# Kernel optimization log

Measured on AMD Instinct MI355X. Metric: run time of the kernel, lower is better.

Reference implementation:

```python
import jax, jax.numpy as jnp
import numpy as np

N = 10000      # num_nodes
E = 80000      # num_edges (no self-loops; added in reference like PyG GATConv)
DIN, DH, DOUT = 768, 256, 64
EPS = 1e-16


def _gat_conv(x, src, dst, W, a_src, a_dst, b, heads, out_ch):
    """PyG-style GATConv (concat=True, negative_slope=0.2, eval mode).
    x: [n, in]; src/dst: [e] (self-loops already included); W: [in, heads*out_ch];
    a_src/a_dst: [heads, out_ch]; b: [heads*out_ch]. Returns [n, heads*out_ch]."""
    n = x.shape[0]
    h = (x @ W).reshape(n, heads, out_ch)                 # [n, H, C]
    e = jax.nn.leaky_relu((h * a_src).sum(-1)[src] + (h * a_dst).sum(-1)[dst],
                          negative_slope=0.2)             # [e, H]
    m = jax.ops.segment_max(e, dst, num_segments=n)       # [n, H]
    m = jnp.where(jnp.isfinite(m), m, 0.0)                # guard empty segments
    p = jnp.exp(e - m[dst])                               # [e, H]
    denom = jax.ops.segment_sum(p, dst, num_segments=n)   # [n, H]
    alpha = p / (denom[dst] + EPS)                        # [e, H]
    msg = h[src] * alpha[:, :, None]                      # [e, H, C]  (largest buffer)
    out = jax.ops.segment_sum(msg, dst, num_segments=n)   # [n, H, C]
    return out.reshape(n, heads * out_ch) + b


def setup_inputs() -> dict:
    key = jax.random.key(0)
    ks = jax.random.split(key, 20)

    def lin(k, fan_in, fan_out):
        return jax.random.normal(k, (fan_in, fan_out), jnp.float32) / np.sqrt(fan_in)

    x = jax.random.normal(ks[0], (N, DIN), jnp.float32)
    src = jax.random.randint(ks[1], (E,), 0, N)
    off = jax.random.randint(ks[2], (E,), 1, N)
    dst = (src + off) % N                                  # guarantees no self-loops
    edge_index = jnp.stack([src, dst]).astype(jnp.int64)

    inp = {"x": x, "edge_index": edge_index}
    inp["W1"]  = lin(ks[3], DIN, 8 * DH)
    inp["as1"] = jax.random.normal(ks[4], (8, DH), jnp.float32) / np.sqrt(DH)
    inp["ad1"] = jax.random.normal(ks[5], (8, DH), jnp.float32) / np.sqrt(DH)
    inp["b1"]  = jnp.zeros((8 * DH,), jnp.float32)
    inp["W2"]  = lin(ks[6], 8 * DH, 4 * DH)
    inp["as2"] = jax.random.normal(ks[7], (4, DH), jnp.float32) / np.sqrt(DH)
    inp["ad2"] = jax.random.normal(ks[8], (4, DH), jnp.float32) / np.sqrt(DH)
    inp["b2"]  = jnp.zeros((4 * DH,), jnp.float32)
    inp["W3"]  = lin(ks[9], 4 * DH, DOUT)
    inp["as3"] = jax.random.normal(ks[10], (1, DOUT), jnp.float32) / np.sqrt(DOUT)
    inp["ad3"] = jax.random.normal(ks[11], (1, DOUT), jnp.float32) / np.sqrt(DOUT)
    inp["b3"]  = jnp.zeros((DOUT,), jnp.float32)
    # reasoning MLP: 64 -> 256 -> 128 -> 1
    inp["r1w"] = lin(ks[12], DOUT, DH);      inp["r1b"] = jnp.zeros((DH,), jnp.float32)
    inp["r2w"] = lin(ks[13], DH, DH // 2);   inp["r2b"] = jnp.zeros((DH // 2,), jnp.float32)
    inp["r3w"] = lin(ks[14], DH // 2, 1);    inp["r3b"] = jnp.zeros((1,), jnp.float32)
    return inp


def reference(x, edge_index, W1, as1, ad1, b1, W2, as2, ad2, b2,
              W3, as3, ad3, b3, r1w, r1b, r2w, r2b, r3w, r3b):
    n = x.shape[0]
    loops = jnp.arange(n, dtype=edge_index.dtype)
    src = jnp.concatenate([edge_index[0], loops])
    dst = jnp.concatenate([edge_index[1], loops])
    # dropout layers are identity in eval mode
    x1 = jax.nn.elu(_gat_conv(x,  src, dst, W1, as1, ad1, b1, 8, DH))
    x2 = jax.nn.elu(_gat_conv(x1, src, dst, W2, as2, ad2, b2, 4, DH))
    x3 = _gat_conv(x2, src, dst, W3, as3, ad3, b3, 1, DOUT)
    h = jax.nn.relu(x3 @ r1w + r1b)
    h = jax.nn.relu(h @ r2w + r2b)
    node_scores = h @ r3w + r3b                            # [n, 1]
    return node_scores, x3
```

## Files before the change

### kernel.cpp

```cpp
#include <hip/hip_runtime.h>
#include <stdint.h>

typedef unsigned short u16;
using s16x8 = __attribute__((ext_vector_type(8))) short;
using f32x4 = __attribute__((ext_vector_type(4))) float;
using u16x8 = __attribute__((ext_vector_type(8))) unsigned short;
using u16x4 = __attribute__((ext_vector_type(4))) unsigned short;

#define DEVINL __device__ __forceinline__

DEVINL float b2f(u16 u) { return __uint_as_float(((uint32_t)u) << 16); }
DEVINL u16 f2b(float f) {
  uint32_t x = __float_as_uint(f);
  return (u16)((x + 0x7fffu + ((x >> 16) & 1u)) >> 16);
}
DEVINL float ldf(const void* p, size_t i, int isbf) {
  return isbf ? b2f(((const u16*)p)[i]) : ((const float*)p)[i];
}
DEVINL void stf(void* p, size_t i, int isbf, float v) {
  if (isbf) ((u16*)p)[i] = f2b(v);
  else      ((float*)p)[i] = v;
}

typedef __attribute__((address_space(1))) const void gvoid;
typedef __attribute__((address_space(3))) void lvoid;
DEVINL void gload_lds16(const u16* g, u16* l) {
  __builtin_amdgcn_global_load_lds((gvoid*)g, (lvoid*)l, 16, 0, 0);
}

constexpr int NN = 10000;
constexpr int NE = 80000;
constexpr int NTOT = 90000;

__global__ void detect_kernel(const void* __restrict__ x, int* __restrict__ flag) {
  int lane = threadIdx.x;
  u16 w = ((const u16*)x)[lane * 97 + 13];
  int e = (w >> 7) & 0xFF;
  int sane = (e >= 0x50 && e <= 0x8A) ? 1 : 0;
  unsigned long long b = __ballot(sane);
  if (lane == 0) flag[0] = (__popcll(b) >= 56) ? 1 : 0;
}

__global__ void cvt_kernel(const void* __restrict__ in, u16* __restrict__ out,
                           int n, const int* __restrict__ FLAG) {
  int isbf = *FLAG;
  int i = blockIdx.x * 256 + threadIdx.x;
  if (i >= n) return;
  out[i] = isbf ? ((const u16*)in)[i] : f2b(((const float*)in)[i]);
}

struct TD { const void* in; u16* out; int R, C, t0; };
struct TD5 { TD d[5]; };
__global__ void transpose_all(TD5 td, const int* __restrict__ FLAG) {
  int isbf = *FLAG;
  __shared__ float tile[32][33];
  int t = blockIdx.x;
  int k = 0;
#pragma unroll
  for (int j = 1; j < 5; j++) if (t >= td.d[j].t0) k = j;
  const void* in = td.d[k].in;
  u16* out = td.d[k].out;
  int R = td.d[k].R, C = td.d[k].C;
  int tl = t - td.d[k].t0;
  int tcols = C / 32;
  int bx = (tl % tcols) * 32, by = (tl / tcols) * 32;
  int tx = threadIdx.x, ty = threadIdx.y;
  for (int j = 0; j < 32; j += 8) {
    int r = by + ty + j, c = bx + tx;
    tile[ty + j][tx] = ldf(in, (size_t)r * C + c, isbf);
  }
  __syncthreads();
  for (int j = 0; j < 32; j += 8) {
    int r = bx + ty + j, c = by + tx;
    out[(size_t)r * R + c] = f2b(tile[tx][ty + j]);
  }
}

__global__ void init_kernel(int* __restrict__ deg, float* __restrict__ hz, int nz) {
  int i = blockIdx.x * blockDim.x + threadIdx.x;
  if (i < NN) deg[i] = 1;
  if (i < nz) hz[i] = 0.f;
}

__global__ void count_deg_kernel(const int* __restrict__ ei, int* __restrict__ deg) {
  int e = blockIdx.x * blockDim.x + threadIdx.x;
  if (e < NE) atomicAdd(&deg[ei[NE + e]], 1);
}

__global__ __launch_bounds__(1024) void scan_kernel(const int* __restrict__ deg,
                                                    int* __restrict__ offs,
                                                    int* __restrict__ cursor, int n) {
  __shared__ int wsum[16];
  __shared__ int carry_s;
  int tid = threadIdx.x, lane = tid & 63, wid = tid >> 6;
  if (tid == 0) carry_s = 0;
  __syncthreads();
  for (int base = 0; base < n; base += 1024) {
    int idx = base + tid;
    int v = (idx < n) ? deg[idx] : 0;
    int s = v;
#pragma unroll
    for (int o = 1; o < 64; o <<= 1) { int t = __shfl_up(s, o); if (lane >= o) s += t; }
    if (lane == 63) wsum[wid] = s;
    __syncthreads();
    if (wid == 0) {
      int w = (lane < 16) ? wsum[lane] : 0;
#pragma unroll
      for (int o = 1; o < 16; o <<= 1) { int t = __shfl_up(w, o); if (lane >= o) w += t; }
      if (lane < 16) wsum[lane] = w;
    }
    __syncthreads();
    int inc = s + (wid > 0 ? wsum[wid - 1] : 0) + carry_s;
    if (idx < n) { offs[idx + 1] = inc; cursor[idx] = inc - v; }
    __syncthreads();
    if (tid == 0) carry_s += wsum[15];
    __syncthreads();
  }
  if (tid == 0) offs[0] = 0;
}

__global__ void scatter_kernel(const int* __restrict__ ei, int* __restrict__ cursor,
                               int* __restrict__ csr_src) {
  int e = blockIdx.x * blockDim.x + threadIdx.x;
  if (e >= NTOT) return;
  int s, d;
  if (e < NE) { s = ei[e]; d = ei[NE + e]; }
  else        { s = e - NE; d = s; }
  int pos = atomicAdd(&cursor[d], 1);
  csr_src[pos] = s;
}

template <int BM, int BN, int WM, int WN>
__global__ __launch_bounds__(256) void gemm_kernel(const u16* __restrict__ A,
                                                   const u16* __restrict__ Bt,
                                                   u16* __restrict__ C,
                                                   int M, int K, int N, int nN,
                                                   const void* __restrict__ bias,
                                                   int do_relu,
                                                   const void* __restrict__ asrc,
                                                   const void* __restrict__ adst,
                                                   float* __restrict__ hs,
                                                   float* __restrict__ hd,
                                                   int H, int Cc,
                                                   const int* __restrict__ FLAG) {
  constexpr int BK = 64;
  constexpr int WTM = BM / WM, WTN = BN / WN;
  constexpr int FM = WTM / 16, FN = WTN / 16;
  constexpr int ACH = BM / 32;
  constexpr int BCH = BN / 32;

  __shared__ u16 smem[(BM + BN) * BK];
  u16* lA = smem;
  u16* lB = smem + BM * BK;

  int tid = threadIdx.x;
  int lane = tid & 63, wid = tid >> 6;
  int wm = wid / WN, wn = wid % WN;
  int isbf = (bias || asrc) ? *FLAG : 0;

  int nwg = gridDim.x;
  int q = nwg >> 3, r = nwg & 7;
  int xcd = blockIdx.x & 7, pos = blockIdx.x >> 3;
  int wgid = (xcd < r ? xcd * (q + 1) : r * (q + 1) + (xcd - r) * q) + pos;
  int bm0 = (wgid / nN) * BM, bn0 = (wgid % nN) * BN;

  int srow = lane >> 3;
  int scol = ((lane & 7) ^ (lane >> 3)) << 3;

  f32x4 acc[FM][FN];
#pragma unroll
  for (int m = 0; m < FM; m++)
#pragma unroll
    for (int n = 0; n < FN; n++) acc[m][n] = (f32x4){0.f, 0.f, 0.f, 0.f};

  for (int k0 = 0; k0 < K; k0 += BK) {
#pragma unroll
    for (int i = 0; i < ACH; i++) {
      int c = wid * ACH + i;
      int row = c * 8 + srow;
      int grow = bm0 + row;
      if (grow > M - 1) grow = M - 1;
      gload_lds16(A + (size_t)grow * K + k0 + scol, lA + c * 512);
    }
#pragma unroll
    for (int i = 0; i < BCH; i++) {
      int c = wid * BCH + i;
      int row = c * 8 + srow;
      gload_lds16(Bt + (size_t)(bn0 + row) * K + k0 + scol, lB + c * 512);
    }
    __syncthreads();

    int swz = (lane & 7) << 4;
#pragma unroll
    for (int ks = 0; ks < 2; ks++) {
      int kb = ks * 64 + ((lane >> 4) << 4);
      s16x8 af[FM], bf[FN];
#pragma unroll
      for (int m = 0; m < FM; m++) {
        int row = wm * WTM + m * 16 + (lane & 15);
        af[m] = *(const s16x8*)((const char*)lA + row * 128 + (kb ^ swz));
      }
#pragma unroll
      for (int n = 0; n < FN; n++) {
        int row = wn * WTN + n * 16 + (lane & 15);
        bf[n] = *(const s16x8*)((const char*)lB + row * 128 + (kb ^ swz));
      }
#pragma unroll
      for (int m = 0; m < FM; m++)
#pragma unroll
        for (int n = 0; n < FN; n++)
          acc[m][n] = __builtin_amdgcn_mfma_f32_16x16x32_bf16(af[m], bf[n], acc[m][n], 0, 0, 0);
    }
    __syncthreads();
  }

  u16* lC = smem;
  int r0 = (lane >> 4) * 4;
  int head = hs ? (bn0 / Cc) : 0;
  int part = hs ? ((bn0 % Cc) / WTN + wn) : 0;
  float asv[FN], adv[FN];
  float sa[FM][4], da[FM][4];
  if (hs) {
#pragma unroll
    for (int n = 0; n < FN; n++) {
      int colC = (bn0 % Cc) + wn * WTN + n * 16 + (lane & 15);
      asv[n] = ldf(asrc, (size_t)head * Cc + colC, isbf);
      adv[n] = ldf(adst, (size_t)head * Cc + colC, isbf);
    }
#pragma unroll
    for (int m = 0; m < FM; m++)
#pragma unroll
      for (int rr = 0; rr < 4; rr++) { sa[m][rr] = 0.f; da[m][rr] = 0.f; }
  }
#pragma unroll
  for (int m = 0; m < FM; m++)
#pragma unroll
    for (int n = 0; n < FN; n++)
#pragma unroll
      for (int rr = 0; rr < 4; rr++) {
        int row = wm * WTM + m * 16 + r0 + rr;
        int col = wn * WTN + n * 16 + (lane & 15);
        float v = acc[m][n][rr];
        if (bias) v += ldf(bias, bn0 + col, isbf);
        if (do_relu) v = fmaxf(v, 0.f);
        if (hs) { sa[m][rr] += v * asv[n]; da[m][rr] += v * adv[n]; }
        lC[row * BN + col] = f2b(v);
      }
  if (hs) {
#pragma unroll
    for (int m = 0; m < FM; m++) {
#pragma unroll
      for (int mask = 1; mask < 16; mask <<= 1)
#pragma unroll
        for (int rr = 0; rr < 4; rr++) {
          sa[m][rr] += __shfl_xor(sa[m][rr], mask);
          da[m][rr] += __shfl_xor(da[m][rr], mask);
        }
      if ((lane & 15) == 0) {
#pragma unroll
        for (int rr = 0; rr < 4; rr++) {
          int grow = bm0 + wm * WTM + m * 16 + r0 + rr;
          if (grow < M) {
            hs[((size_t)grow * H + head) * 4 + part] = sa[m][rr];
            hd[((size_t)grow * H + head) * 4 + part] = da[m][rr];
          }
        }
      }
    }
  }
  if (C) {
    __syncthreads();
    constexpr int CHUNKS = BM * BN / 2048;
    constexpr int CPR = BN / 8;
#pragma unroll
    for (int j = 0; j < CHUNKS; j++) {
      int idx = j * 256 + tid;
      int row = idx / CPR, colb = (idx % CPR) * 16;
      int grow = bm0 + row;
      if (grow < M) {
        int4 v = *(const int4*)((const char*)lC + idx * 16);
        *(int4*)((char*)C + ((size_t)grow * N + bn0) * 2 + colb) = v;
      }
    }
  }
}

template <int HC, int VPT, int TPB, int H, int ECAP>
__global__ __launch_bounds__(TPB) void agg_fused_kernel(
    const u16* __restrict__ h, const float* __restrict__ hs, const float* __restrict__ hd,
    const int* __restrict__ csr_src, const int* __restrict__ offs,
    const void* __restrict__ bias, u16* __restrict__ outb, void* __restrict__ outv,
    int do_elu, const int* __restrict__ FLAG) {
  constexpr int C = HC / H;
  constexpr int CH = 64;
  int isbf = *FLAG;
  int i = blockIdx.x;
  int t = threadIdx.x;
  int p0 = offs[i], p1 = offs[i + 1];
  int deg = p1 - p0;
  __shared__ float m_s[H], inv_s[H], hd_s[H];
  __shared__ float lalpha[ECAP * H];
  __shared__ int lsrc[ECAP];
  const float4* hs4 = (const float4*)hs;

  if (t < H) {
    float4 qd = ((const float4*)hd)[(size_t)i * H + t];
    hd_s[t] = (qd.x + qd.y) + (qd.z + qd.w);
  }
  __syncthreads();

  int hh = (t >> 5) % H, j = t & 31;
  bool crew = (t < H * 32);
  int c0 = t * VPT;
  int head = c0 / C;
  float acc[VPT];
#pragma unroll
  for (int v = 0; v < VPT; v++) acc[v] = 0.f;

  if (deg <= ECAP) {
    for (int idx = t; idx < deg; idx += TPB) lsrc[idx] = csr_src[p0 + idx];
    if (crew) {
      float hdv = hd_s[hh];
      float mm = -1e30f;
      for (int idx = j; idx < deg; idx += 32) {
        float4 qv = hs4[(size_t)csr_src[p0 + idx] * H + hh];
        float e = (qv.x + qv.y) + (qv.z + qv.w) + hdv;
        e = e > 0.f ? e : 0.2f * e;
        lalpha[idx * H + hh] = e;
        mm = fmaxf(mm, e);
      }
#pragma unroll
      for (int msk = 16; msk; msk >>= 1) mm = fmaxf(mm, __shfl_xor(mm, msk));
      float dd = 0.f;
      for (int idx = j; idx < deg; idx += 32) {
        float v = __expf(lalpha[idx * H + hh] - mm);
        lalpha[idx * H + hh] = v;
        dd += v;
      }
#pragma unroll
      for (int msk = 16; msk; msk >>= 1) dd += __shfl_xor(dd, msk);
      float inv = 1.f / (dd + 1e-16f);
      for (int idx = j; idx < deg; idx += 32)
        lalpha[idx * H + hh] *= inv;
    }
    __syncthreads();

    int p = 0;
    for (; p + 4 <= deg; p += 4) {
      int s0 = lsrc[p], s1 = lsrc[p + 1], s2 = lsrc[p + 2], s3 = lsrc[p + 3];
      float a0 = lalpha[p * H + head];
      float a1 = lalpha[(p + 1) * H + head];
      float a2 = lalpha[(p + 2) * H + head];
      float a3 = lalpha[(p + 3) * H + head];
      const u16* h0 = h + (size_t)s0 * HC + c0;
      const u16* h1 = h + (size_t)s1 * HC + c0;
      const u16* h2 = h + (size_t)s2 * HC + c0;
      const u16* h3 = h + (size_t)s3 * HC + c0;
      if constexpr (VPT == 8) {
        u16x8 v0 = *(const u16x8*)h0, v1 = *(const u16x8*)h1;
        u16x8 v2 = *(const u16x8*)h2, v3 = *(const u16x8*)h3;
#pragma unroll
        for (int v = 0; v < 8; v++)
          acc[v] += (a0 * b2f(v0[v]) + a1 * b2f(v1[v])) + (a2 * b2f(v2[v]) + a3 * b2f(v3[v]));
      } else if constexpr (VPT == 4) {
        u16x4 v0 = *(const u16x4*)h0, v1 = *(const u16x4*)h1;
        u16x4 v2 = *(const u16x4*)h2, v3 = *(const u16x4*)h3;
#pragma unroll
        for (int v = 0; v < 4; v++)
          acc[v] += (a0 * b2f(v0[v]) + a1 * b2f(v1[v])) + (a2 * b2f(v2[v]) + a3 * b2f(v3[v]));
      } else {
        acc[0] += (a0 * b2f(h0[0]) + a1 * b2f(h1[0])) + (a2 * b2f(h2[0]) + a3 * b2f(h3[0]));
      }
    }
    for (; p < deg; ++p) {
      int s0 = lsrc[p];
      float a0 = lalpha[p * H + head];
      const u16* h0 = h + (size_t)s0 * HC + c0;
      if constexpr (VPT == 8) {
        u16x8 v0 = *(const u16x8*)h0;
#pragma unroll
        for (int v = 0; v < 8; v++) acc[v] += a0 * b2f(v0[v]);
      } else if constexpr (VPT == 4) {
        u16x4 v0 = *(const u16x4*)h0;
#pragma unroll
        for (int v = 0; v < 4; v++) acc[v] += a0 * b2f(v0[v]);
      } else {
        acc[0] += a0 * b2f(h0[0]);
      }
    }
  } else {
    if (crew) {
      float hdv = hd_s[hh];
      float mm = -1e30f;
      for (int p = p0 + j; p < p1; p += 32) {
        float4 qv = hs4[(size_t)csr_src[p] * H + hh];
        float e = (qv.x + qv.y) + (qv.z + qv.w) + hdv;
        e = e > 0.f ? e : 0.2f * e;
        mm = fmaxf(mm, e);
      }
#pragma unroll
      for (int msk = 16; msk; msk >>= 1) mm = fmaxf(mm, __shfl_xor(mm, msk));
      float dd = 0.f;
      for (int p = p0 + j; p < p1; p += 32) {
        float4 qv = hs4[(size_t)csr_src[p] * H + hh];
        float e = (qv.x + qv.y) + (qv.z + qv.w) + hdv;
        e = e > 0.f ? e : 0.2f * e;
        dd += __expf(e - mm);
      }
#pragma unroll
      for (int msk = 16; msk; msk >>= 1) dd += __shfl_xor(dd, msk);
      if (j == 0) { m_s[hh] = mm; inv_s[hh] = 1.f / (dd + 1e-16f); }
    }
    for (int base = p0; base < p1; base += CH) {
      int cend = base + CH < p1 ? base + CH : p1;
      __syncthreads();
      if (crew) {
        float hdv = hd_s[hh];
        float mmv = m_s[hh], inv = inv_s[hh];
        for (int p = base + j; p < cend; p += 32) {
          float4 qv = hs4[(size_t)csr_src[p] * H + hh];
          float e = (qv.x + qv.y) + (qv.z + qv.w) + hdv;
          e = e > 0.f ? e : 0.2f * e;
          lalpha[(p - base) * H + hh] = __expf(e - mmv) * inv;
        }
      }
      if (t < cend - base) lsrc[t] = csr_src[base + t];
      __syncthreads();
      for (int p = base; p < cend; ++p) {
        int s0 = lsrc[p - base];
        float a0 = lalpha[(p - base) * H + head];
        const u16* h0 = h + (size_t)s0 * HC + c0;
        if constexpr (VPT == 8) {
          u16x8 v0 = *(const u16x8*)h0;
#pragma unroll
          for (int v = 0; v < 8; v++) acc[v] += a0 * b2f(v0[v]);
        } else if constexpr (VPT == 4) {
          u16x4 v0 = *(const u16x4*)h0;
#pragma unroll
          for (int v = 0; v < 4; v++) acc[v] += a0 * b2f(v0[v]);
        } else {
          acc[0] += a0 * b2f(h0[0]);
        }
      }
    }
  }

  float r[VPT];
#pragma unroll
  for (int v = 0; v < VPT; v++) {
    r[v] = acc[v] + ldf(bias, c0 + v, isbf);
    if (do_elu) r[v] = r[v] > 0.f ? r[v] : expm1f(r[v]);
  }
  if (outb) {
    if constexpr (VPT == 8) {
      u16x8 o;
#pragma unroll
      for (int v = 0; v < 8; v++) o[v] = f2b(r[v]);
      *(u16x8*)(outb + (size_t)i * HC + c0) = o;
    } else if constexpr (VPT == 4) {
      u16x4 o;
#pragma unroll
      for (int v = 0; v < 4; v++) o[v] = f2b(r[v]);
      *(u16x4*)(outb + (size_t)i * HC + c0) = o;
    } else {
      outb[(size_t)i * HC + c0] = f2b(r[0]);
    }
  }
  if (outv) {
#pragma unroll
    for (int v = 0; v < VPT; v++)
      stf(outv, (size_t)10000 + (size_t)i * HC + c0 + v, isbf, r[v]);
  }
}

__global__ void scores_kernel(const float* __restrict__ sc, const void* __restrict__ r3b,
                              void* __restrict__ scores, const int* __restrict__ FLAG) {
  int isbf = *FLAG;
  int i = blockIdx.x * 256 + threadIdx.x;
  if (i >= NN) return;
  float4 q = ((const float4*)sc)[i];
  stf(scores, i, isbf, (q.x + q.y) + (q.z + q.w) + ldf(r3b, 0, isbf));
}

extern "C" void kernel_launch(void* const* d_in, const int* in_sizes, int n_in,
                              void* d_out, int out_size, void* d_ws, size_t ws_size,
                              hipStream_t stream) {
  const void* x   = d_in[0];
  const int* ei   = (const int*)d_in[1];
  const void* W1  = d_in[2];
  const void* as1 = d_in[3];
  const void* ad1 = d_in[4];
  const void* b1  = d_in[5];
  const void* W2  = d_in[6];
  const void* as2 = d_in[7];
  const void* ad2 = d_in[8];
  const void* b2  = d_in[9];
  const void* W3  = d_in[10];
  const void* as3 = d_in[11];
  const void* ad3 = d_in[12];
  const void* b3  = d_in[13];
  const void* r1w = d_in[14];
  const void* r1b = d_in[15];
  const void* r2w = d_in[16];
  const void* r2b = d_in[17];
  const void* r3w = d_in[18];
  const void* r3b = d_in[19];

  char* ws = (char*)d_ws;
  size_t o = 0;
  auto alloc = [&](size_t bytes) { void* p = ws + o; o += (bytes + 255) & ~(size_t)255; return p; };
  u16* XC     = (u16*)alloc((size_t)NN * 768 * 2);
  u16* W1T    = (u16*)alloc((size_t)2048 * 768 * 2);
  u16* W2T    = (u16*)alloc((size_t)1024 * 2048 * 2);
  u16* W3T    = (u16*)alloc((size_t)64 * 1024 * 2);
  u16* R1T    = (u16*)alloc((size_t)256 * 64 * 2);
  u16* R2T    = (u16*)alloc((size_t)128 * 256 * 2);
  u16* Hbuf   = (u16*)alloc((size_t)NN * 2048 * 2);
  u16* Xbuf   = (u16*)alloc((size_t)NN * 2048 * 2);
  u16* X3B    = (u16*)alloc((size_t)NN * 64 * 2);
  u16* H1B    = (u16*)alloc((size_t)NN * 256 * 2);
  float* HZ   = (float*)alloc((size_t)NN * 112 * 4);
  float* HS1  = HZ;
  float* HD1  = HZ + (size_t)NN * 32;
  float* HS2  = HZ + (size_t)NN * 64;
  float* HD2  = HZ + (size_t)NN * 80;
  float* HS3  = HZ + (size_t)NN * 96;
  float* HD3  = HZ + (size_t)NN * 100;
  float* SC   = HZ + (size_t)NN * 104;
  float* SD   = HZ + (size_t)NN * 108;
  int* DEG    = (int*)alloc((size_t)NN * 4);
  int* OFFS   = (int*)alloc((size_t)(NN + 1) * 4);
  int* CURSOR = (int*)alloc((size_t)NN * 4);
  int* CSR    = (int*)alloc((size_t)NTOT * 4);
  int* FLAG   = (int*)alloc(256);

  detect_kernel<<<1, 64, 0, stream>>>(x, FLAG);
  cvt_kernel<<<(NN * 768 + 255) / 256, 256, 0, stream>>>(x, XC, NN * 768, FLAG);

  TD5 td;
  td.d[0] = {W1,  W1T, 768, 2048, 0};
  td.d[1] = {W2,  W2T, 2048, 1024, 0};
  td.d[2] = {W3,  W3T, 1024, 64, 0};
  td.d[3] = {r1w, R1T, 64, 256, 0};
  td.d[4] = {r2w, R2T, 256, 128, 0};
  int cum = 0;
  for (int k = 0; k < 5; k++) {
    td.d[k].t0 = cum;
    cum += (td.d[k].R / 32) * (td.d[k].C / 32);
  }
  transpose_all<<<cum, dim3(32, 8), 0, stream>>>(td, FLAG);

  init_kernel<<<(NN * 112 + 255) / 256, 256, 0, stream>>>(DEG, HZ, NN * 112);
  count_deg_kernel<<<(NE + 255) / 256, 256, 0, stream>>>(ei, DEG);
  scan_kernel<<<1, 1024, 0, stream>>>(DEG, OFFS, CURSOR, NN);
  scatter_kernel<<<(NTOT + 255) / 256, 256, 0, stream>>>(ei, CURSOR, CSR);

  const int MT = (NN + 127) / 128;
  const int MT64 = (NN + 63) / 64;

  gemm_kernel<64, 128, 2, 2><<<MT64 * 16, 256, 0, stream>>>(
      XC, W1T, Hbuf, NN, 768, 2048, 16, nullptr, 0, as1, ad1, HS1, HD1, 8, 256, FLAG);
  agg_fused_kernel<2048, 8, 256, 8, 512><<<NN, 256, 0, stream>>>(
      Hbuf, HS1, HD1, CSR, OFFS, b1, Xbuf, nullptr, 1, FLAG);

  gemm_kernel<64, 128, 2, 2><<<MT64 * 8, 256, 0, stream>>>(
      Xbuf, W2T, Hbuf, NN, 2048, 1024, 8, nullptr, 0, as2, ad2, HS2, HD2, 4, 256, FLAG);
  agg_fused_kernel<1024, 4, 256, 4, 512><<<NN, 256, 0, stream>>>(
      Hbuf, HS2, HD2, CSR, OFFS, b2, Xbuf, nullptr, 1, FLAG);

  gemm_kernel<128, 64, 4, 1><<<MT, 256, 0, stream>>>(
      Xbuf, W3T, Hbuf, NN, 1024, 64, 1, nullptr, 0, as3, ad3, HS3, HD3, 1, 64, FLAG);
  agg_fused_kernel<64, 1, 64, 1, 512><<<NN, 64, 0, stream>>>(
      Hbuf, HS3, HD3, CSR, OFFS, b3, X3B, d_out, 0, FLAG);

  gemm_kernel<64, 64, 2, 2><<<MT64 * 4, 256, 0, stream>>>(
      X3B, R1T, H1B, NN, 64, 256, 4, r1b, 1, nullptr, nullptr, nullptr, nullptr, 0, 0, FLAG);
  gemm_kernel<64, 64, 2, 2><<<MT64 * 2, 256, 0, stream>>>(
      H1B, R2T, nullptr, NN, 256, 128, 2, r2b, 1, r3w, r3w, SC, SD, 1, 128, FLAG);
  scores_kernel<<<(NN + 255) / 256, 256, 0, stream>>>(SC, r3b, d_out, FLAG);
}
```

Measured before the change: 337.6 us.

## Widen per-thread vector width in GAT aggregation, shrink LDS, fold dtype detect into convert

```diff
diff --git a/kernel.cpp b/kernel.cpp
--- a/kernel.cpp
+++ b/kernel.cpp
@@ -32,21 +32,21 @@
 constexpr int NE = 80000;
 constexpr int NTOT = 90000;
 
-__global__ void detect_kernel(const void* __restrict__ x, int* __restrict__ flag) {
-  int lane = threadIdx.x;
-  u16 w = ((const u16*)x)[lane * 97 + 13];
-  int e = (w >> 7) & 0xFF;
-  int sane = (e >= 0x50 && e <= 0x8A) ? 1 : 0;
-  unsigned long long b = __ballot(sane);
-  if (lane == 0) flag[0] = (__popcll(b) >= 56) ? 1 : 0;
-}
-
 __global__ void cvt_kernel(const void* __restrict__ in, u16* __restrict__ out,
-                           int n, const int* __restrict__ FLAG) {
-  int isbf = *FLAG;
+                           int n, int* __restrict__ flagout) {
+  __shared__ int sflag;
+  if (threadIdx.x < 64) {
+    u16 w = ((const u16*)in)[threadIdx.x * 97 + 13];
+    int e = (w >> 7) & 0xFF;
+    int sane = (e >= 0x50 && e <= 0x8A) ? 1 : 0;
+    unsigned long long b = __ballot(sane);
+    if (threadIdx.x == 0) sflag = (__popcll(b) >= 56) ? 1 : 0;
+  }
+  __syncthreads();
+  int isbf = sflag;
   int i = blockIdx.x * 256 + threadIdx.x;
-  if (i >= n) return;
-  out[i] = isbf ? ((const u16*)in)[i] : f2b(((const float*)in)[i]);
+  if (i < n) out[i] = isbf ? ((const u16*)in)[i] : f2b(((const float*)in)[i]);
+  if (blockIdx.x == 0 && threadIdx.x == 0) flagout[0] = isbf;
 }
 
 struct TD { const void* in; u16* out; int R, C, t0; };
@@ -292,6 +292,8 @@
     const void* __restrict__ bias, u16* __restrict__ outb, void* __restrict__ outv,
     int do_elu, const int* __restrict__ FLAG) {
   constexpr int C = HC / H;
+  constexpr int L = (TPB / H) < 64 ? (TPB / H) : 64;
+  constexpr int PH = H + 1;
   constexpr int CH = 64;
   int isbf = *FLAG;
   int i = blockIdx.x;
@@ -299,7 +301,7 @@
   int p0 = offs[i], p1 = offs[i + 1];
   int deg = p1 - p0;
   __shared__ float m_s[H], inv_s[H], hd_s[H];
-  __shared__ float lalpha[ECAP * H];
+  __shared__ float lalpha[ECAP * PH];
   __shared__ int lsrc[ECAP];
   const float4* hs4 = (const float4*)hs;
 
@@ -309,8 +311,8 @@
   }
   __syncthreads();
 
-  int hh = (t >> 5) % H, j = t & 31;
-  bool crew = (t < H * 32);
+  int hh = (t / L) % H, j = t % L;
+  bool crew = (t < H * L);
   int c0 = t * VPT;
   int head = c0 / C;
   float acc[VPT];
@@ -322,93 +324,121 @@
     if (crew) {
       float hdv = hd_s[hh];
       float mm = -1e30f;
-      for (int idx = j; idx < deg; idx += 32) {
+      for (int idx = j; idx < deg; idx += L) {
         float4 qv = hs4[(size_t)csr_src[p0 + idx] * H + hh];
         float e = (qv.x + qv.y) + (qv.z + qv.w) + hdv;
         e = e > 0.f ? e : 0.2f * e;
-        lalpha[idx * H + hh] = e;
+        lalpha[idx * PH + hh] = e;
         mm = fmaxf(mm, e);
       }
 #pragma unroll
-      for (int msk = 16; msk; msk >>= 1) mm = fmaxf(mm, __shfl_xor(mm, msk));
+      for (int msk = L / 2; msk; msk >>= 1) mm = fmaxf(mm, __shfl_xor(mm, msk));
       float dd = 0.f;
-      for (int idx = j; idx < deg; idx += 32) {
-        float v = __expf(lalpha[idx * H + hh] - mm);
-        lalpha[idx * H + hh] = v;
+      for (int idx = j; idx < deg; idx += L) {
+        float v = __expf(lalpha[idx * PH + hh] - mm);
+        lalpha[idx * PH + hh] = v;
         dd += v;
       }
 #pragma unroll
-      for (int msk = 16; msk; msk >>= 1) dd += __shfl_xor(dd, msk);
+      for (int msk = L / 2; msk; msk >>= 1) dd += __shfl_xor(dd, msk);
       float inv = 1.f / (dd + 1e-16f);
-      for (int idx = j; idx < deg; idx += 32)
-        lalpha[idx * H + hh] *= inv;
+      for (int idx = j; idx < deg; idx += L)
+        lalpha[idx * PH + hh] *= inv;
     }
     __syncthreads();
 
     int p = 0;
-    for (; p + 4 <= deg; p += 4) {
-      int s0 = lsrc[p], s1 = lsrc[p + 1], s2 = lsrc[p + 2], s3 = lsrc[p + 3];
-      float a0 = lalpha[p * H + head];
-      float a1 = lalpha[(p + 1) * H + head];
-      float a2 = lalpha[(p + 2) * H + head];
-      float a3 = lalpha[(p + 3) * H + head];
-      const u16* h0 = h + (size_t)s0 * HC + c0;
-      const u16* h1 = h + (size_t)s1 * HC + c0;
-      const u16* h2 = h + (size_t)s2 * HC + c0;
-      const u16* h3 = h + (size_t)s3 * HC + c0;
-      if constexpr (VPT == 8) {
-        u16x8 v0 = *(const u16x8*)h0, v1 = *(const u16x8*)h1;
-        u16x8 v2 = *(const u16x8*)h2, v3 = *(const u16x8*)h3;
-#pragma unroll
-        for (int v = 0; v < 8; v++)
-          acc[v] += (a0 * b2f(v0[v]) + a1 * b2f(v1[v])) + (a2 * b2f(v2[v]) + a3 * b2f(v3[v]));
-      } else if constexpr (VPT == 4) {
-        u16x4 v0 = *(const u16x4*)h0, v1 = *(const u16x4*)h1;
-        u16x4 v2 = *(const u16x4*)h2, v3 = *(const u16x4*)h3;
-#pragma unroll
-        for (int v = 0; v < 4; v++)
-          acc[v] += (a0 * b2f(v0[v]) + a1 * b2f(v1[v])) + (a2 * b2f(v2[v]) + a3 * b2f(v3[v]));
-      } else {
-        acc[0] += (a0 * b2f(h0[0]) + a1 * b2f(h1[0])) + (a2 * b2f(h2[0]) + a3 * b2f(h3[0]));
-      }
-    }
-    for (; p < deg; ++p) {
-      int s0 = lsrc[p];
-      float a0 = lalpha[p * H + head];
-      const u16* h0 = h + (size_t)s0 * HC + c0;
-      if constexpr (VPT == 8) {
-        u16x8 v0 = *(const u16x8*)h0;
-#pragma unroll
-        for (int v = 0; v < 8; v++) acc[v] += a0 * b2f(v0[v]);
-      } else if constexpr (VPT == 4) {
-        u16x4 v0 = *(const u16x4*)h0;
-#pragma unroll
-        for (int v = 0; v < 4; v++) acc[v] += a0 * b2f(v0[v]);
-      } else {
-        acc[0] += a0 * b2f(h0[0]);
+    if constexpr (VPT == 16) {
+      for (; p + 2 <= deg; p += 2) {
+        int s0 = lsrc[p], s1 = lsrc[p + 1];
+        float a0 = lalpha[p * PH + head];
+        float a1 = lalpha[(p + 1) * PH + head];
+        const u16* h0 = h + (size_t)s0 * HC + c0;
+        const u16* h1 = h + (size_t)s1 * HC + c0;
+        u16x8 va0 = *(const u16x8*)h0, vb0 = *(const u16x8*)(h0 + 8);
+        u16x8 va1 = *(const u16x8*)h1, vb1 = *(const u16x8*)(h1 + 8);
+#pragma unroll
+        for (int v = 0; v < 8; v++) {
+          acc[v] += a0 * b2f(va0[v]) + a1 * b2f(va1[v]);
+          acc[8 + v] += a0 * b2f(vb0[v]) + a1 * b2f(vb1[v]);
+        }
+      }
+      for (; p < deg; ++p) {
+        int s0 = lsrc[p];
+        float a0 = lalpha[p * PH + head];
+        const u16* h0 = h + (size_t)s0 * HC + c0;
+        u16x8 va0 = *(const u16x8*)h0, vb0 = *(const u16x8*)(h0 + 8);
+#pragma unroll
+        for (int v = 0; v < 8; v++) {
+          acc[v] += a0 * b2f(va0[v]);
+          acc[8 + v] += a0 * b2f(vb0[v]);
+        }
+      }
+    } else {
+      for (; p + 4 <= deg; p += 4) {
+        int s0 = lsrc[p], s1 = lsrc[p + 1], s2 = lsrc[p + 2], s3 = lsrc[p + 3];
+        float a0 = lalpha[p * PH + head];
+        float a1 = lalpha[(p + 1) * PH + head];
+        float a2 = lalpha[(p + 2) * PH + head];
+        float a3 = lalpha[(p + 3) * PH + head];
+        const u16* h0 = h + (size_t)s0 * HC + c0;
+        const u16* h1 = h + (size_t)s1 * HC + c0;
+        const u16* h2 = h + (size_t)s2 * HC + c0;
+        const u16* h3 = h + (size_t)s3 * HC + c0;
+        if constexpr (VPT == 8) {
+          u16x8 v0 = *(const u16x8*)h0, v1 = *(const u16x8*)h1;
+          u16x8 v2 = *(const u16x8*)h2, v3 = *(const u16x8*)h3;
+#pragma unroll
+          for (int v = 0; v < 8; v++)
+            acc[v] += (a0 * b2f(v0[v]) + a1 * b2f(v1[v])) + (a2 * b2f(v2[v]) + a3 * b2f(v3[v]));
+        } else if constexpr (VPT == 4) {
+          u16x4 v0 = *(const u16x4*)h0, v1 = *(const u16x4*)h1;
+          u16x4 v2 = *(const u16x4*)h2, v3 = *(const u16x4*)h3;
+#pragma unroll
+          for (int v = 0; v < 4; v++)
+            acc[v] += (a0 * b2f(v0[v]) + a1 * b2f(v1[v])) + (a2 * b2f(v2[v]) + a3 * b2f(v3[v]));
+        } else {
+          acc[0] += (a0 * b2f(h0[0]) + a1 * b2f(h1[0])) + (a2 * b2f(h2[0]) + a3 * b2f(h3[0]));
+        }
+      }
+      for (; p < deg; ++p) {
+        int s0 = lsrc[p];
+        float a0 = lalpha[p * PH + head];
+        const u16* h0 = h + (size_t)s0 * HC + c0;
+        if constexpr (VPT == 8) {
+          u16x8 v0 = *(const u16x8*)h0;
+#pragma unroll
+          for (int v = 0; v < 8; v++) acc[v] += a0 * b2f(v0[v]);
+        } else if constexpr (VPT == 4) {
+          u16x4 v0 = *(const u16x4*)h0;
+#pragma unroll
+          for (int v = 0; v < 4; v++) acc[v] += a0 * b2f(v0[v]);
+        } else {
+          acc[0] += a0 * b2f(h0[0]);
+        }
       }
     }
   } else {
     if (crew) {
       float hdv = hd_s[hh];
       float mm = -1e30f;
-      for (int p = p0 + j; p < p1; p += 32) {
+      for (int p = p0 + j; p < p1; p += L) {
         float4 qv = hs4[(size_t)csr_src[p] * H + hh];
         float e = (qv.x + qv.y) + (qv.z + qv.w) + hdv;
         e = e > 0.f ? e : 0.2f * e;
         mm = fmaxf(mm, e);
       }
 #pragma unroll
-      for (int msk = 16; msk; msk >>= 1) mm = fmaxf(mm, __shfl_xor(mm, msk));
+      for (int msk = L / 2; msk; msk >>= 1) mm = fmaxf(mm, __shfl_xor(mm, msk));
       float dd = 0.f;
-      for (int p = p0 + j; p < p1; p += 32) {
+      for (int p = p0 + j; p < p1; p += L) {
         float4 qv = hs4[(size_t)csr_src[p] * H + hh];
         float e = (qv.x + qv.y) + (qv.z + qv.w) + hdv;
         e = e > 0.f ? e : 0.2f * e;
         dd += __expf(e - mm);
       }
 #pragma unroll
-      for (int msk = 16; msk; msk >>= 1) dd += __shfl_xor(dd, msk);
+      for (int msk = L / 2; msk; msk >>= 1) dd += __shfl_xor(dd, msk);
       if (j == 0) { m_s[hh] = mm; inv_s[hh] = 1.f / (dd + 1e-16f); }
     }
     for (int base = p0; base < p1; base += CH) {
@@ -417,20 +447,27 @@
       if (crew) {
         float hdv = hd_s[hh];
         float mmv = m_s[hh], inv = inv_s[hh];
-        for (int p = base + j; p < cend; p += 32) {
+        for (int p = base + j; p < cend; p += L) {
           float4 qv = hs4[(size_t)csr_src[p] * H + hh];
           float e = (qv.x + qv.y) + (qv.z + qv.w) + hdv;
           e = e > 0.f ? e : 0.2f * e;
-          lalpha[(p - base) * H + hh] = __expf(e - mmv) * inv;
-        }
-      }
-      if (t < cend - base) lsrc[t] = csr_src[base + t];
+          lalpha[(p - base) * PH + hh] = __expf(e - mmv) * inv;
+        }
+      }
+      for (int idx = t; idx < cend - base; idx += TPB) lsrc[idx] = csr_src[base + idx];
       __syncthreads();
       for (int p = base; p < cend; ++p) {
         int s0 = lsrc[p - base];
-        float a0 = lalpha[(p - base) * H + head];
+        float a0 = lalpha[(p - base) * PH + head];
         const u16* h0 = h + (size_t)s0 * HC + c0;
-        if constexpr (VPT == 8) {
+        if constexpr (VPT == 16) {
+          u16x8 va = *(const u16x8*)h0, vb = *(const u16x8*)(h0 + 8);
+#pragma unroll
+          for (int v = 0; v < 8; v++) {
+            acc[v] += a0 * b2f(va[v]);
+            acc[8 + v] += a0 * b2f(vb[v]);
+          }
+        } else if constexpr (VPT == 8) {
           u16x8 v0 = *(const u16x8*)h0;
 #pragma unroll
           for (int v = 0; v < 8; v++) acc[v] += a0 * b2f(v0[v]);
@@ -452,7 +489,13 @@
     if (do_elu) r[v] = r[v] > 0.f ? r[v] : expm1f(r[v]);
   }
   if (outb) {
-    if constexpr (VPT == 8) {
+    if constexpr (VPT == 16) {
+      u16x8 oa, ob;
+#pragma unroll
+      for (int v = 0; v < 8; v++) { oa[v] = f2b(r[v]); ob[v] = f2b(r[8 + v]); }
+      *(u16x8*)(outb + (size_t)i * HC + c0) = oa;
+      *(u16x8*)(outb + (size_t)i * HC + c0 + 8) = ob;
+    } else if constexpr (VPT == 8) {
       u16x8 o;
 #pragma unroll
       for (int v = 0; v < 8; v++) o[v] = f2b(r[v]);
@@ -534,7 +577,6 @@
   int* CSR    = (int*)alloc((size_t)NTOT * 4);
   int* FLAG   = (int*)alloc(256);
 
-  detect_kernel<<<1, 64, 0, stream>>>(x, FLAG);
   cvt_kernel<<<(NN * 768 + 255) / 256, 256, 0, stream>>>(x, XC, NN * 768, FLAG);
 
   TD5 td;
@@ -560,17 +602,17 @@
 
   gemm_kernel<64, 128, 2, 2><<<MT64 * 16, 256, 0, stream>>>(
       XC, W1T, Hbuf, NN, 768, 2048, 16, nullptr, 0, as1, ad1, HS1, HD1, 8, 256, FLAG);
-  agg_fused_kernel<2048, 8, 256, 8, 512><<<NN, 256, 0, stream>>>(
+  agg_fused_kernel<2048, 16, 128, 8, 96><<<NN, 128, 0, stream>>>(
       Hbuf, HS1, HD1, CSR, OFFS, b1, Xbuf, nullptr, 1, FLAG);
 
   gemm_kernel<64, 128, 2, 2><<<MT64 * 8, 256, 0, stream>>>(
       Xbuf, W2T, Hbuf, NN, 2048, 1024, 8, nullptr, 0, as2, ad2, HS2, HD2, 4, 256, FLAG);
-  agg_fused_kernel<1024, 4, 256, 4, 512><<<NN, 256, 0, stream>>>(
+  agg_fused_kernel<1024, 8, 128, 4, 96><<<NN, 128, 0, stream>>>(
       Hbuf, HS2, HD2, CSR, OFFS, b2, Xbuf, nullptr, 1, FLAG);
 
   gemm_kernel<128, 64, 4, 1><<<MT, 256, 0, stream>>>(
       Xbuf, W3T, Hbuf, NN, 1024, 64, 1, nullptr, 0, as3, ad3, HS3, HD3, 1, 64, FLAG);
-  agg_fused_kernel<64, 1, 64, 1, 512><<<NN, 64, 0, stream>>>(
+  agg_fused_kernel<64, 1, 64, 1, 96><<<NN, 64, 0, stream>>>(
       Hbuf, HS3, HD3, CSR, OFFS, b3, X3B, d_out, 0, FLAG);
 
   gemm_kernel<64, 64, 2, 2><<<MT64 * 4, 256, 0, stream>>>(
```

Result: no change. 339.9 us (+0.7%).
